# Kernel tuning notes

Hardware: AMD Instinct MI355X
Metric: run time of the kernel (lower is better)

Reference implementation:

```python
import jax, jax.numpy as jnp
import numpy as np

E, HEADS, HD, L, FF = 768, 12, 64, 12, 3072


def layernorm(x, g, b, eps=1e-5):
    m = jnp.mean(x, axis=-1, keepdims=True)
    v = jnp.var(x, axis=-1, keepdims=True)
    return (x - m) / jnp.sqrt(v + eps) * g + b


def setup_inputs() -> dict:
    key = jax.random.key(0)
    ks = jax.random.split(key, 26)
    B, N, PS = 32, 1024, 24
    P2 = PS * PS
    def rn(k, shape, s=0.02):
        return jax.random.normal(k, shape, dtype=jnp.float32) * s
    return {
        "scene_masks": jax.random.normal(ks[0], (B, N, PS, PS), dtype=jnp.float32),
        "target_mask": jax.random.normal(ks[1], (B, PS, PS), dtype=jnp.float32),
        "emb_W": rn(ks[2], (E, P2)),            # torch Linear weight [out,in]
        "emb_b": rn(ks[3], (E,)),
        "class_embed": rn(ks[4], (1, 1, E)),
        "scene_pos": rn(ks[5], (1, N + 1, E)),
        "target_pos": rn(ks[6], (1, 2, E)),
        "ln1_g": jnp.ones((L, E), jnp.float32),
        "ln1_b": jnp.zeros((L, E), jnp.float32),
        "ln2_g": jnp.ones((L, E), jnp.float32),
        "ln2_b": jnp.zeros((L, E), jnp.float32),
        "Wq": rn(ks[7], (L, HD, HD)),
        "Wk": rn(ks[8], (L, HD, HD)),
        "Wv": rn(ks[9], (L, HD, HD)),
        "Wo": rn(ks[10], (L, E, E)),
        "bo": rn(ks[11], (L, E)),
        "W1": rn(ks[12], (L, FF, E)),
        "b1": rn(ks[13], (L, FF)),
        "W2": rn(ks[14], (L, E, FF)),
        "b2": rn(ks[15], (L, E)),
        "mlp_W": rn(ks[16], (N, E)),
        "mlp_b": rn(ks[17], (N,)),
    }


def _forward_logits(scene_masks, target_mask, emb_W, emb_b, class_embed, scene_pos,
                    target_pos, ln1_g, ln1_b, ln2_g, ln2_b, Wq, Wk, Wv, Wo, bo,
                    W1, b1, W2, b2, mlp_W, mlp_b):
    B, N, H, W = scene_masks.shape
    P2 = H * W
    scene = scene_masks.reshape(B, N, P2) @ emb_W.T + emb_b          # [B,N,E]
    tgt = target_mask.reshape(B, 1, P2) @ emb_W.T + emb_b            # [B,1,E]
    cls = jnp.broadcast_to(class_embed, (B, 1, E))
    scene = jnp.concatenate([cls, scene], axis=1) + scene_pos[:, :N + 1]  # [B,N+1,E]
    tgt = jnp.concatenate([cls, tgt], axis=1) + target_pos               # [B,2,E]
    scale = jnp.sqrt(jnp.float32(E))

    def block(tq, p):
        g1, bb1n, g2, bb2n, wq, wk, wv, wo, bo_, w1, b1_, w2, b2_ = p
        kv = layernorm(scene, g1, bb1n)                # norm1(value)=norm1(key)
        q = layernorm(tq, g1, bb1n)                    # norm1(query)
        kvh = kv.reshape(B, N + 1, HEADS, HD)
        qh = q.reshape(B, 2, HEADS, HD)
        # per-head Linear shares one [HD,HD] weight across all heads
        qs = jnp.einsum('nqhd,ed->nqhe', qh, wq)
        ks_ = jnp.einsum('nkhd,ed->nkhe', kvh, wk)
        vs = jnp.einsum('nkhd,ed->nkhe', kvh, wv)
        energy = jnp.einsum('nqhd,nkhd->nhqk', qs, ks_)     # [B,H,2,N+1]
        att = jax.nn.softmax(energy / scale, axis=-1)
        out = jnp.einsum('nhqk,nkhd->nqhd', att, vs).reshape(B, 2, E)
        out = out @ wo.T + bo_
        x = layernorm(out + tq, g1, bb1n)
        ff = jax.nn.relu(x @ w1.T + b1_) @ w2.T + b2_
        return layernorm(ff + x, g2, bb2n), None

    params = (ln1_g, ln1_b, ln2_g, ln2_b, Wq, Wk, Wv, Wo, bo, W1, b1, W2, b2)
    tgt, _ = jax.lax.scan(block, tgt, params)
    x = jnp.mean(tgt, axis=1) @ mlp_W.T + mlp_b       # [B, num_patches]
    return x


def reference(scene_masks, target_mask, emb_W, emb_b, class_embed, scene_pos,
              target_pos, ln1_g, ln1_b, ln2_g, ln2_b, Wq, Wk, Wv, Wo, bo,
              W1, b1, W2, b2, mlp_W, mlp_b):
    x = _forward_logits(scene_masks, target_mask, emb_W, emb_b, class_embed,
                        scene_pos, target_pos, ln1_g, ln1_b, ln2_g, ln2_b,
                        Wq, Wk, Wv, Wo, bo, W1, b1, W2, b2, mlp_W, mlp_b)
    # sorted_nodes = argsort desc + 1; eye(P+1)[nodes-1] == one_hot(argsort desc)
    order = jnp.argsort(-x, axis=1)[:, :5]                # top-5 patch indices
    return jax.nn.one_hot(order, x.shape[1] + 1, dtype=jnp.float32)  # [B,5,P+1]
```

## Files before the change

kernel.cpp:

```cpp
#include <hip/hip_runtime.h>
#include <math.h>

#define E_DIM 768
#define NTOK 1025
#define B_DIM 32
#define NHEADS 12
#define HDIM 64
#define LAYERS 12
#define FF_DIM 3072
#define P2 576

__device__ __forceinline__ float block_reduce_sum(float v, float* red) {
  int tid = threadIdx.x;
  red[tid] = v;
  __syncthreads();
#pragma unroll
  for (int s = 128; s > 0; s >>= 1) {
    if (tid < s) red[tid] += red[tid + s];
    __syncthreads();
  }
  float r = red[0];
  __syncthreads();
  return r;
}

__global__ __launch_bounds__(256) void embed_gemm(
    const float* __restrict__ A, const float* __restrict__ W,
    const float* __restrict__ bias, const float* __restrict__ pos,
    float* __restrict__ scene) {
  __shared__ float Xs[16][132];
  __shared__ float Ws[16][132];
  int tid = threadIdx.x;
  int n0 = blockIdx.x * 128;
  int m0 = blockIdx.y * 128;
  int lr = tid >> 2;
  int lk = (tid & 3) << 2;
  int ty = tid >> 4, tx = tid & 15;
  float acc[8][8] = {};
  for (int k0 = 0; k0 < P2; k0 += 16) {
    float4 x0 = *(const float4*)(A + (size_t)(m0 + lr) * P2 + k0 + lk);
    float4 x1 = *(const float4*)(A + (size_t)(m0 + 64 + lr) * P2 + k0 + lk);
    float4 w0 = *(const float4*)(W + (size_t)(n0 + lr) * P2 + k0 + lk);
    float4 w1 = *(const float4*)(W + (size_t)(n0 + 64 + lr) * P2 + k0 + lk);
    __syncthreads();
    Xs[lk + 0][lr] = x0.x; Xs[lk + 1][lr] = x0.y; Xs[lk + 2][lr] = x0.z; Xs[lk + 3][lr] = x0.w;
    Xs[lk + 0][64 + lr] = x1.x; Xs[lk + 1][64 + lr] = x1.y; Xs[lk + 2][64 + lr] = x1.z; Xs[lk + 3][64 + lr] = x1.w;
    Ws[lk + 0][lr] = w0.x; Ws[lk + 1][lr] = w0.y; Ws[lk + 2][lr] = w0.z; Ws[lk + 3][lr] = w0.w;
    Ws[lk + 0][64 + lr] = w1.x; Ws[lk + 1][64 + lr] = w1.y; Ws[lk + 2][64 + lr] = w1.z; Ws[lk + 3][64 + lr] = w1.w;
    __syncthreads();
#pragma unroll
    for (int kk = 0; kk < 16; ++kk) {
      float4 a0 = *(const float4*)&Xs[kk][ty << 2];
      float4 a1 = *(const float4*)&Xs[kk][64 + (ty << 2)];
      float4 b0 = *(const float4*)&Ws[kk][tx << 2];
      float4 b1 = *(const float4*)&Ws[kk][64 + (tx << 2)];
      float av[8] = {a0.x, a0.y, a0.z, a0.w, a1.x, a1.y, a1.z, a1.w};
      float bv[8] = {b0.x, b0.y, b0.z, b0.w, b1.x, b1.y, b1.z, b1.w};
#pragma unroll
      for (int i = 0; i < 8; ++i)
#pragma unroll
        for (int j = 0; j < 8; ++j) acc[i][j] += av[i] * bv[j];
    }
  }
#pragma unroll
  for (int i = 0; i < 8; ++i) {
    int mloc = (i < 4) ? ((ty << 2) + i) : (64 + (ty << 2) + i - 4);
    int m = m0 + mloc;
    int b = m >> 10, nt = m & 1023;
    size_t row = ((size_t)b * NTOK + 1 + nt) * E_DIM;
    size_t prow = (size_t)(1 + nt) * E_DIM;
#pragma unroll
    for (int half = 0; half < 2; ++half) {
      int n = n0 + half * 64 + (tx << 2);
      float4 o4;
      o4.x = acc[i][half * 4 + 0] + bias[n + 0] + pos[prow + n + 0];
      o4.y = acc[i][half * 4 + 1] + bias[n + 1] + pos[prow + n + 1];
      o4.z = acc[i][half * 4 + 2] + bias[n + 2] + pos[prow + n + 2];
      o4.w = acc[i][half * 4 + 3] + bias[n + 3] + pos[prow + n + 3];
      *(float4*)&scene[row + n] = o4;
    }
  }
}

__global__ void scene_cls(const float* __restrict__ cls, const float* __restrict__ pos,
                          float* __restrict__ scene) {
  int b = blockIdx.x;
  for (int e = threadIdx.x; e < E_DIM; e += 256)
    scene[(size_t)b * NTOK * E_DIM + e] = cls[e] + pos[e];
}

__global__ __launch_bounds__(256) void ln_rows(const float* __restrict__ in, float* __restrict__ out) {
  __shared__ float red[256];
  int r = blockIdx.x, tid = threadIdx.x;
  const float* x = in + (size_t)r * E_DIM;
  float a0 = x[tid], a1 = x[tid + 256], a2 = x[tid + 512];
  float mean = block_reduce_sum(a0 + a1 + a2, red) * (1.f / 768.f);
  float d0 = a0 - mean, d1 = a1 - mean, d2 = a2 - mean;
  float var = block_reduce_sum(d0 * d0 + d1 * d1 + d2 * d2, red) * (1.f / 768.f);
  float rinv = rsqrtf(var + 1e-5f);
  float* o = out + (size_t)r * E_DIM;
  o[tid] = d0 * rinv; o[tid + 256] = d1 * rinv; o[tid + 512] = d2 * rinv;
}

__global__ __launch_bounds__(256) void tgt_init(
    const float* __restrict__ tmask, const float* __restrict__ W,
    const float* __restrict__ bias, const float* __restrict__ cls,
    const float* __restrict__ tpos, float* __restrict__ tq) {
  int b = blockIdx.x, tid = threadIdx.x;
  for (int e = tid; e < E_DIM; e += 256)
    tq[(size_t)(b * 2) * E_DIM + e] = cls[e] + tpos[e];
  const float* tm = tmask + (size_t)b * P2;
  for (int e = tid; e < E_DIM; e += 256) {
    const float* wr = W + (size_t)e * P2;
    float s = 0.f;
    for (int k = 0; k < P2; k += 4) {
      float4 w4 = *(const float4*)&wr[k];
      float4 t4 = *(const float4*)&tm[k];
      s += w4.x * t4.x + w4.y * t4.y + w4.z * t4.z + w4.w * t4.w;
    }
    tq[(size_t)(b * 2 + 1) * E_DIM + e] = s + bias[e] + tpos[E_DIM + e];
  }
}

__global__ void prep_m(const float* __restrict__ Wq, const float* __restrict__ Wk,
                       float* __restrict__ Mb) {
  int l = blockIdx.y;
  int idx = blockIdx.x * 256 + threadIdx.x;
  int d = idx >> 6, dp = idx & 63;
  const float* wq = Wq + l * 4096;
  const float* wk = Wk + l * 4096;
  float s = 0.f;
#pragma unroll 8
  for (int e = 0; e < 64; ++e) s += wq[e * 64 + d] * wk[e * 64 + dp];
  Mb[l * 4096 + idx] = s;
}

__global__ void prep_wvo(const float* __restrict__ Wv, const float* __restrict__ Wo,
                         float* __restrict__ Wvo) {
  int l = blockIdx.y;
  int idx = blockIdx.x * 256 + threadIdx.x;
  int ep = idx / 768, hd = idx % 768;
  int h = hd >> 6, d = hd & 63;
  const float* wv = Wv + (size_t)l * 4096;
  const float* wo = Wo + (size_t)l * 768 * 768 + (size_t)ep * 768 + h * 64;
  float s = 0.f;
#pragma unroll 8
  for (int ev = 0; ev < 64; ++ev) s += wv[ev * 64 + d] * wo[ev];
  Wvo[(size_t)l * 589824 + idx] = s;
}

#define ACH 272
__global__ __launch_bounds__(256) void attn_flash_q(
    const float* __restrict__ tq, const float* __restrict__ Mb,
    const float* __restrict__ g1, const float* __restrict__ b1, int l,
    const float* __restrict__ ns, float* __restrict__ ctx) {
  __shared__ float red[256];
  __shared__ float qs[2][64];
  __shared__ float qg[2][64];
  __shared__ float qmb[2];
  __shared__ float sred[2][16];
  __shared__ float cred[2][16][64];
  int b = blockIdx.x / NHEADS;
  int h = blockIdx.x % NHEADS;
  int tid = threadIdx.x;
  const float* gl = g1 + l * E_DIM;
  const float* bl = b1 + l * E_DIM;
  int seg = h >> 2;
  int base = h * 64 - seg * 256;
  for (int r = 0; r < 2; ++r) {
    const float* x = tq + (size_t)(b * 2 + r) * E_DIM;
    float a0 = x[tid], a1 = x[tid + 256], a2 = x[tid + 512];
    float mean = block_reduce_sum(a0 + a1 + a2, red) * (1.f / 768.f);
    float d0 = a0 - mean, d1 = a1 - mean, d2 = a2 - mean;
    float var = block_reduce_sum(d0 * d0 + d1 * d1 + d2 * d2, red) * (1.f / 768.f);
    float rinv = rsqrtf(var + 1e-5f);
    float dv = (seg == 0) ? d0 : ((seg == 1) ? d1 : d2);
    if (tid >= base && tid < base + 64) {
      int d = tid - base;
      qs[r][d] = dv * rinv * gl[h * 64 + d] + bl[h * 64 + d];
    }
  }
  __syncthreads();
  const float inv_scale = rsqrtf(768.f);
  if (tid < 128) {
    int r = tid >> 6, dp = tid & 63;
    const float* M = Mb + l * 4096;
    float s = 0.f;
#pragma unroll 8
    for (int d = 0; d < 64; ++d) s += qs[r][d] * M[d * 64 + dp];
    qg[r][dp] = s * gl[h * 64 + dp] * inv_scale;
    red[tid] = s * bl[h * 64 + dp];
  }
  __syncthreads();
  if (tid < 2) {
    float a = 0.f;
    for (int dp = 0; dp < 64; ++dp) a += red[tid * 64 + dp];
    qmb[tid] = a * inv_scale;
  }
  __syncthreads();
  int g = tid >> 4;
  int lane = tid & 15;
  int r0 = b * 2, r1 = r0 + 1;
  const float* nsb = ns + (size_t)b * NTOK * E_DIM + h * 64;
  float4 q0v = *(const float4*)&qg[0][lane * 4];
  float4 q1v = *(const float4*)&qg[1][lane * 4];
  float qb0 = qmb[0], qb1 = qmb[1];
  float m = -1e30f, s0 = 0.f, s1 = 0.f;
  float4 c0 = {0, 0, 0, 0}, c1 = {0, 0, 0, 0};
  float4 v[17];
  float e0a[17], e1a[17];
  for (int cb = 0; cb < NTOK; cb += ACH) {
    int ntk = NTOK - cb; if (ntk > ACH) ntk = ACH;
    int cnt = (ntk - g + 15) >> 4;
    float mloc = -1e30f;
#pragma unroll
    for (int i = 0; i < 17; ++i) {
      if (i < cnt) {
        int k = cb + g + (i << 4);
        float4 vv = *(const float4*)(nsb + (size_t)k * E_DIM + lane * 4);
        v[i] = vv;
        float p0 = vv.x * q0v.x + vv.y * q0v.y + vv.z * q0v.z + vv.w * q0v.w;
        float p1 = vv.x * q1v.x + vv.y * q1v.y + vv.z * q1v.z + vv.w * q1v.w;
#pragma unroll
        for (int off = 8; off; off >>= 1) {
          p0 += __shfl_xor(p0, off, 16);
          p1 += __shfl_xor(p1, off, 16);
        }
        float e0 = p0 + qb0, e1 = p1 + qb1;
        e0a[i] = e0; e1a[i] = e1;
        mloc = fmaxf(mloc, fmaxf(e0, e1));
      }
    }
    red[tid] = mloc;
    __syncthreads();
#pragma unroll
    for (int s = 128; s > 0; s >>= 1) {
      if (tid < s) red[tid] = fmaxf(red[tid], red[tid + s]);
      __syncthreads();
    }
    float mnew = fmaxf(m, red[0]);
    __syncthreads();
    if (mnew > m) {
      float f = expf(m - mnew);
      s0 *= f; s1 *= f;
      c0.x *= f; c0.y *= f; c0.z *= f; c0.w *= f;
      c1.x *= f; c1.y *= f; c1.z *= f; c1.w *= f;
      m = mnew;
    }
#pragma unroll
    for (int i = 0; i < 17; ++i) {
      if (i < cnt) {
        float p0 = expf(e0a[i] - m);
        float p1 = expf(e1a[i] - m);
        s0 += p0; s1 += p1;
        c0.x += p0 * v[i].x; c0.y += p0 * v[i].y; c0.z += p0 * v[i].z; c0.w += p0 * v[i].w;
        c1.x += p1 * v[i].x; c1.y += p1 * v[i].y; c1.z += p1 * v[i].z; c1.w += p1 * v[i].w;
      }
    }
  }
  if (lane == 0) { sred[0][g] = s0; sred[1][g] = s1; }
  *(float4*)&cred[0][g][lane * 4] = c0;
  *(float4*)&cred[1][g][lane * 4] = c1;
  __syncthreads();
  if (tid < 128) {
    int t = tid >> 6, dd = tid & 63;
    int o = h * 64 + dd;
    float stot = 0.f, cs = 0.f;
#pragma unroll
    for (int gg = 0; gg < 16; ++gg) { stot += sred[t][gg]; cs += cred[t][gg][dd]; }
    float inv = 1.f / stot;
    ctx[(size_t)(r0 + t) * E_DIM + o] = cs * inv * gl[o] + bl[o];
  }
}

__global__ __launch_bounds__(256) void skinny_part(
    const float* __restrict__ X, int K, const float* __restrict__ W,
    int kchunk, float* __restrict__ part, int N) {
  __shared__ float Xs[16][64];
  __shared__ float Ws[16][64];
  int tid = threadIdx.x;
  int n0 = blockIdx.x * 64;
  int s = blockIdx.y;
  int kbeg = s * kchunk;
  int lr = tid >> 2;
  int lk = (tid & 3) << 2;
  int ty = tid >> 4, tx = tid & 15;
  float acc[4][4] = {};
  for (int k0 = kbeg; k0 < kbeg + kchunk; k0 += 16) {
    float4 xv = *(const float4*)(X + (size_t)lr * K + k0 + lk);
    float4 wv = *(const float4*)(W + (size_t)(n0 + lr) * K + k0 + lk);
    __syncthreads();
    Xs[lk + 0][lr] = xv.x; Xs[lk + 1][lr] = xv.y; Xs[lk + 2][lr] = xv.z; Xs[lk + 3][lr] = xv.w;
    Ws[lk + 0][lr] = wv.x; Ws[lk + 1][lr] = wv.y; Ws[lk + 2][lr] = wv.z; Ws[lk + 3][lr] = wv.w;
    __syncthreads();
#pragma unroll
    for (int kk = 0; kk < 16; ++kk) {
      float4 a4 = *(const float4*)&Xs[kk][ty << 2];
      float4 b4 = *(const float4*)&Ws[kk][tx << 2];
      float av[4] = {a4.x, a4.y, a4.z, a4.w};
      float bv[4] = {b4.x, b4.y, b4.z, b4.w};
#pragma unroll
      for (int i = 0; i < 4; ++i)
#pragma unroll
        for (int j = 0; j < 4; ++j) acc[i][j] += av[i] * bv[j];
    }
  }
#pragma unroll
  for (int i = 0; i < 4; ++i) {
    int mm = (ty << 2) + i;
    float4 o4 = make_float4(acc[i][0], acc[i][1], acc[i][2], acc[i][3]);
    *(float4*)&part[((size_t)s * 64 + mm) * N + n0 + (tx << 2)] = o4;
  }
}

__global__ __launch_bounds__(256) void skinny_h1_part(
    const float* __restrict__ part1, const float* __restrict__ b1,
    const float* __restrict__ W, int kchunk, float* __restrict__ part2) {
  __shared__ float Xs[16][64];
  __shared__ float Ws[16][64];
  const int K = 3072, N = 768;
  int tid = threadIdx.x;
  int n0 = blockIdx.x * 64;
  int s = blockIdx.y;
  int kbeg = s * kchunk;
  int lr = tid >> 2;
  int lk = (tid & 3) << 2;
  int ty = tid >> 4, tx = tid & 15;
  float acc[4][4] = {};
  for (int k0 = kbeg; k0 < kbeg + kchunk; k0 += 16) {
    float4 x0 = *(const float4*)(part1 + (size_t)lr * K + k0 + lk);
    float4 x1 = *(const float4*)(part1 + (size_t)(64 + lr) * K + k0 + lk);
    float4 x2 = *(const float4*)(part1 + (size_t)(128 + lr) * K + k0 + lk);
    float4 x3 = *(const float4*)(part1 + (size_t)(192 + lr) * K + k0 + lk);
    float4 bb = *(const float4*)(b1 + k0 + lk);
    float4 xv;
    xv.x = fmaxf(x0.x + x1.x + x2.x + x3.x + bb.x, 0.f);
    xv.y = fmaxf(x0.y + x1.y + x2.y + x3.y + bb.y, 0.f);
    xv.z = fmaxf(x0.z + x1.z + x2.z + x3.z + bb.z, 0.f);
    xv.w = fmaxf(x0.w + x1.w + x2.w + x3.w + bb.w, 0.f);
    float4 wv = *(const float4*)(W + (size_t)(n0 + lr) * K + k0 + lk);
    __syncthreads();
    Xs[lk + 0][lr] = xv.x; Xs[lk + 1][lr] = xv.y; Xs[lk + 2][lr] = xv.z; Xs[lk + 3][lr] = xv.w;
    Ws[lk + 0][lr] = wv.x; Ws[lk + 1][lr] = wv.y; Ws[lk + 2][lr] = wv.z; Ws[lk + 3][lr] = wv.w;
    __syncthreads();
#pragma unroll
    for (int kk = 0; kk < 16; ++kk) {
      float4 a4 = *(const float4*)&Xs[kk][ty << 2];
      float4 b4 = *(const float4*)&Ws[kk][tx << 2];
      float av[4] = {a4.x, a4.y, a4.z, a4.w};
      float bv[4] = {b4.x, b4.y, b4.z, b4.w};
#pragma unroll
      for (int i = 0; i < 4; ++i)
#pragma unroll
        for (int j = 0; j < 4; ++j) acc[i][j] += av[i] * bv[j];
    }
  }
#pragma unroll
  for (int i = 0; i < 4; ++i) {
    int mm = (ty << 2) + i;
    float4 o4 = make_float4(acc[i][0], acc[i][1], acc[i][2], acc[i][3]);
    *(float4*)&part2[((size_t)s * 64 + mm) * N + n0 + (tx << 2)] = o4;
  }
}

__global__ __launch_bounds__(256) void reduce_ln(
    const float* __restrict__ part, int S, const float* __restrict__ bias,
    const float* __restrict__ res, const float* __restrict__ g,
    const float* __restrict__ bsh, float* __restrict__ out,
    float* __restrict__ xmean) {
  __shared__ float red[256];
  int m = blockIdx.x, tid = threadIdx.x;
  float t[3];
#pragma unroll
  for (int c = 0; c < 3; ++c) {
    int n = tid + c * 256;
    float s = 0.f;
    for (int i = 0; i < S; ++i) s += part[((size_t)i * 64 + m) * 768 + n];
    t[c] = s + bias[n] + res[(size_t)m * 768 + n];
  }
  float mean = block_reduce_sum(t[0] + t[1] + t[2], red) * (1.f / 768.f);
  float d0 = t[0] - mean, d1 = t[1] - mean, d2 = t[2] - mean;
  float var = block_reduce_sum(d0 * d0 + d1 * d1 + d2 * d2, red) * (1.f / 768.f);
  float rinv = rsqrtf(var + 1e-5f);
  float y0 = d0 * rinv * g[tid] + bsh[tid];
  float y1 = d1 * rinv * g[tid + 256] + bsh[tid + 256];
  float y2 = d2 * rinv * g[tid + 512] + bsh[tid + 512];
  out[(size_t)m * 768 + tid] = y0;
  out[(size_t)m * 768 + tid + 256] = y1;
  out[(size_t)m * 768 + tid + 512] = y2;
  if (xmean) {
    float* xr = xmean + (size_t)(m >> 1) * 768;
    atomicAdd(&xr[tid], 0.5f * y0);
    atomicAdd(&xr[tid + 256], 0.5f * y1);
    atomicAdd(&xr[tid + 512], 0.5f * y2);
  }
}

__global__ __launch_bounds__(256) void top5_from_parts(
    const float* __restrict__ part, const float* __restrict__ bias,
    float* __restrict__ out) {
  __shared__ float v[1024];
  __shared__ float bv[256];
  __shared__ int bi[256];
  int b = blockIdx.x, tid = threadIdx.x;
  for (int i = tid; i < 1024; i += 256) {
    float s = part[(size_t)(0 * 64 + b) * 1024 + i] + part[(size_t)(1 * 64 + b) * 1024 + i] +
              part[(size_t)(2 * 64 + b) * 1024 + i] + part[(size_t)(3 * 64 + b) * 1024 + i];
    v[i] = s + bias[i];
  }
  float* ob = out + (size_t)b * 5 * NTOK;
  for (int i = tid; i < 5 * NTOK; i += 256) ob[i] = 0.f;
  __syncthreads();
  for (int it = 0; it < 5; ++it) {
    float best = -1e38f;
    int bidx = 0x7fffffff;
    for (int i = tid; i < 1024; i += 256) {
      float x = v[i];
      if (x > best || (x == best && i < bidx)) { best = x; bidx = i; }
    }
    bv[tid] = best; bi[tid] = bidx;
    __syncthreads();
    for (int s = 128; s > 0; s >>= 1) {
      if (tid < s) {
        if (bv[tid + s] > bv[tid] || (bv[tid + s] == bv[tid] && bi[tid + s] < bi[tid])) {
          bv[tid] = bv[tid + s]; bi[tid] = bi[tid + s];
        }
      }
      __syncthreads();
    }
    if (tid == 0) {
      ob[it * NTOK + bi[0]] = 1.0f;
      v[bi[0]] = -1e38f;
    }
    __syncthreads();
  }
}

extern "C" void kernel_launch(void* const* d_in, const int* in_sizes, int n_in,
                              void* d_out, int out_size, void* d_ws, size_t ws_size,
                              hipStream_t stream) {
  const float* scene_masks = (const float*)d_in[0];
  const float* target_mask = (const float*)d_in[1];
  const float* emb_W = (const float*)d_in[2];
  const float* emb_b = (const float*)d_in[3];
  const float* class_embed = (const float*)d_in[4];
  const float* scene_pos = (const float*)d_in[5];
  const float* target_pos = (const float*)d_in[6];
  const float* ln1_g = (const float*)d_in[7];
  const float* ln1_b = (const float*)d_in[8];
  const float* ln2_g = (const float*)d_in[9];
  const float* ln2_b = (const float*)d_in[10];
  const float* Wq = (const float*)d_in[11];
  const float* Wk = (const float*)d_in[12];
  const float* Wv = (const float*)d_in[13];
  const float* Wo = (const float*)d_in[14];
  const float* bo = (const float*)d_in[15];
  const float* W1 = (const float*)d_in[16];
  const float* fb1 = (const float*)d_in[17];
  const float* W2 = (const float*)d_in[18];
  const float* fb2 = (const float*)d_in[19];
  const float* mlp_W = (const float*)d_in[20];
  const float* mlp_b = (const float*)d_in[21];
  float* out = (float*)d_out;

  float* ws = (float*)d_ws;
  float* scene = ws;
  float* Mbuf = scene + 25190400;
  float* Wvo = Mbuf + 49152;
  float* tq = Wvo + 7077888;
  float* ctxf = tq + 49152;
  float* xbuf = ctxf + 49152;
  float* xm = xbuf + 49152;
  float* partA = xm + 49152;
  float* partB = partA + 786432;

  embed_gemm<<<dim3(6, 256), 256, 0, stream>>>(scene_masks, emb_W, emb_b, scene_pos, scene);
  scene_cls<<<32, 256, 0, stream>>>(class_embed, scene_pos, scene);
  ln_rows<<<32 * NTOK, 256, 0, stream>>>(scene, scene);
  tgt_init<<<32, 256, 0, stream>>>(target_mask, emb_W, emb_b, class_embed, target_pos, tq);
  prep_m<<<dim3(16, 12), 256, 0, stream>>>(Wq, Wk, Mbuf);
  prep_wvo<<<dim3(2304, 12), 256, 0, stream>>>(Wv, Wo, Wvo);
  hipMemsetAsync(xm, 0, 49152 * sizeof(float), stream);

  for (int l = 0; l < LAYERS; ++l) {
    attn_flash_q<<<32 * NHEADS, 256, 0, stream>>>(tq, Mbuf, ln1_g, ln1_b, l, scene, ctxf);
    skinny_part<<<dim3(12, 8), 256, 0, stream>>>(ctxf, 768, Wvo + (size_t)l * 589824, 96, partA, 768);
    reduce_ln<<<64, 256, 0, stream>>>(partA, 8, bo + l * 768, tq,
                                      ln1_g + l * 768, ln1_b + l * 768, xbuf, nullptr);
    skinny_part<<<dim3(48, 4), 256, 0, stream>>>(xbuf, 768, W1 + (size_t)l * FF_DIM * 768, 192, partB, FF_DIM);
    skinny_h1_part<<<dim3(12, 16), 256, 0, stream>>>(partB, fb1 + l * FF_DIM,
                                                     W2 + (size_t)l * 768 * FF_DIM, 192, partA);
    reduce_ln<<<64, 256, 0, stream>>>(partA, 16, fb2 + l * 768, xbuf,
                                      ln2_g + l * 768, ln2_b + l * 768, tq,
                                      (l == LAYERS - 1) ? xm : nullptr);
  }

  skinny_part<<<dim3(16, 4), 256, 0, stream>>>(xm, 768, mlp_W, 192, partA, 1024);
  top5_from_parts<<<32, 256, 0, stream>>>(partA, mlp_b, out);
}
```

Baseline: 1.931 ms.

## Fuse Wvo projection into attention and replace split-K partials with atomic accumulators

The attention kernel now projects its per-head context through the combined Wvo matrix itself and atomically adds the result into an accumulator. That accumulator is pre-seeded with the residual plus output bias. The second FFN GEMM also accumulates with atomics into a buffer pre-seeded with the residual plus bias. This removes one skinny GEMM launch per layer and the partial-sum reduction passes. In exchange it adds atomic contention, makes float summation order nondeterministic, and has each attention block re-read a slice of Wvo.

```diff
diff --git a/kernel.cpp b/kernel.cpp
--- a/kernel.cpp
+++ b/kernel.cpp
@@ -105,10 +105,14 @@
 __global__ __launch_bounds__(256) void tgt_init(
     const float* __restrict__ tmask, const float* __restrict__ W,
     const float* __restrict__ bias, const float* __restrict__ cls,
-    const float* __restrict__ tpos, float* __restrict__ tq) {
+    const float* __restrict__ tpos, const float* __restrict__ bo0,
+    float* __restrict__ tq, float* __restrict__ acc1) {
   int b = blockIdx.x, tid = threadIdx.x;
-  for (int e = tid; e < E_DIM; e += 256)
-    tq[(size_t)(b * 2) * E_DIM + e] = cls[e] + tpos[e];
+  for (int e = tid; e < E_DIM; e += 256) {
+    float v = cls[e] + tpos[e];
+    tq[(size_t)(b * 2) * E_DIM + e] = v;
+    acc1[(size_t)(b * 2) * E_DIM + e] = v + bo0[e];
+  }
   const float* tm = tmask + (size_t)b * P2;
   for (int e = tid; e < E_DIM; e += 256) {
     const float* wr = W + (size_t)e * P2;
@@ -118,7 +122,9 @@
       float4 t4 = *(const float4*)&tm[k];
       s += w4.x * t4.x + w4.y * t4.y + w4.z * t4.z + w4.w * t4.w;
     }
-    tq[(size_t)(b * 2 + 1) * E_DIM + e] = s + bias[e] + tpos[E_DIM + e];
+    float v = s + bias[e] + tpos[E_DIM + e];
+    tq[(size_t)(b * 2 + 1) * E_DIM + e] = v;
+    acc1[(size_t)(b * 2 + 1) * E_DIM + e] = v + bo0[e];
   }
 }
 
@@ -153,13 +159,15 @@
 __global__ __launch_bounds__(256) void attn_flash_q(
     const float* __restrict__ tq, const float* __restrict__ Mb,
     const float* __restrict__ g1, const float* __restrict__ b1, int l,
-    const float* __restrict__ ns, float* __restrict__ ctx) {
+    const float* __restrict__ ns, const float* __restrict__ Wvo_l,
+    float* __restrict__ acc1) {
   __shared__ float red[256];
   __shared__ float qs[2][64];
   __shared__ float qg[2][64];
   __shared__ float qmb[2];
   __shared__ float sred[2][16];
   __shared__ float cred[2][16][64];
+  __shared__ float ctxs[2][64];
   int b = blockIdx.x / NHEADS;
   int h = blockIdx.x % NHEADS;
   int tid = threadIdx.x;
@@ -269,8 +277,49 @@
 #pragma unroll
     for (int gg = 0; gg < 16; ++gg) { stot += sred[t][gg]; cs += cred[t][gg][dd]; }
     float inv = 1.f / stot;
-    ctx[(size_t)(r0 + t) * E_DIM + o] = cs * inv * gl[o] + bl[o];
-  }
+    ctxs[t][dd] = cs * inv * gl[o] + bl[o];
+  }
+  __syncthreads();
+  const float* wbase = Wvo_l + (size_t)h * 64 + lane * 4;
+  float4 x0 = *(const float4*)&ctxs[0][lane * 4];
+  float4 x1 = *(const float4*)&ctxs[1][lane * 4];
+  for (int n = g; n < 768; n += 16) {
+    float4 wv = *(const float4*)(wbase + (size_t)n * 768);
+    float a0 = wv.x * x0.x + wv.y * x0.y + wv.z * x0.z + wv.w * x0.w;
+    float a1 = wv.x * x1.x + wv.y * x1.y + wv.z * x1.z + wv.w * x1.w;
+#pragma unroll
+    for (int off = 8; off; off >>= 1) {
+      a0 += __shfl_xor(a0, off, 16);
+      a1 += __shfl_xor(a1, off, 16);
+    }
+    if (lane == 0) {
+      atomicAdd(&acc1[(size_t)r0 * E_DIM + n], a0);
+      atomicAdd(&acc1[(size_t)r1 * E_DIM + n], a1);
+    }
+  }
+}
+
+__global__ __launch_bounds__(256) void ln1_ff2init(
+    const float* __restrict__ acc1, const float* __restrict__ g,
+    const float* __restrict__ bsh, const float* __restrict__ fb2l,
+    float* __restrict__ x, float* __restrict__ acc2) {
+  __shared__ float red[256];
+  int m = blockIdx.x, tid = threadIdx.x;
+  const float* a = acc1 + (size_t)m * E_DIM;
+  float t0 = a[tid], t1 = a[tid + 256], t2 = a[tid + 512];
+  float mean = block_reduce_sum(t0 + t1 + t2, red) * (1.f / 768.f);
+  float d0 = t0 - mean, d1 = t1 - mean, d2 = t2 - mean;
+  float var = block_reduce_sum(d0 * d0 + d1 * d1 + d2 * d2, red) * (1.f / 768.f);
+  float rinv = rsqrtf(var + 1e-5f);
+  float y0 = d0 * rinv * g[tid] + bsh[tid];
+  float y1 = d1 * rinv * g[tid + 256] + bsh[tid + 256];
+  float y2 = d2 * rinv * g[tid + 512] + bsh[tid + 512];
+  x[(size_t)m * E_DIM + tid] = y0;
+  x[(size_t)m * E_DIM + tid + 256] = y1;
+  x[(size_t)m * E_DIM + tid + 512] = y2;
+  acc2[(size_t)m * E_DIM + tid] = y0 + fb2l[tid];
+  acc2[(size_t)m * E_DIM + tid + 256] = y1 + fb2l[tid + 256];
+  acc2[(size_t)m * E_DIM + tid + 512] = y2 + fb2l[tid + 512];
 }
 
 __global__ __launch_bounds__(256) void skinny_part(
@@ -313,9 +362,9 @@
   }
 }
 
-__global__ __launch_bounds__(256) void skinny_h1_part(
+__global__ __launch_bounds__(256) void skinny_h1_atomic(
     const float* __restrict__ part1, const float* __restrict__ b1,
-    const float* __restrict__ W, int kchunk, float* __restrict__ part2) {
+    const float* __restrict__ W, int kchunk, float* __restrict__ acc2) {
   __shared__ float Xs[16][64];
   __shared__ float Ws[16][64];
   const int K = 3072, N = 768;
@@ -358,38 +407,40 @@
 #pragma unroll
   for (int i = 0; i < 4; ++i) {
     int mm = (ty << 2) + i;
-    float4 o4 = make_float4(acc[i][0], acc[i][1], acc[i][2], acc[i][3]);
-    *(float4*)&part2[((size_t)s * 64 + mm) * N + n0 + (tx << 2)] = o4;
-  }
-}
-
-__global__ __launch_bounds__(256) void reduce_ln(
-    const float* __restrict__ part, int S, const float* __restrict__ bias,
-    const float* __restrict__ res, const float* __restrict__ g,
-    const float* __restrict__ bsh, float* __restrict__ out,
+    float* dst = acc2 + (size_t)mm * N + n0 + (tx << 2);
+    atomicAdd(dst + 0, acc[i][0]);
+    atomicAdd(dst + 1, acc[i][1]);
+    atomicAdd(dst + 2, acc[i][2]);
+    atomicAdd(dst + 3, acc[i][3]);
+  }
+}
+
+__global__ __launch_bounds__(256) void ln2_next(
+    const float* __restrict__ acc2, const float* __restrict__ g,
+    const float* __restrict__ bsh, const float* __restrict__ bo_next,
+    float* __restrict__ tq, float* __restrict__ acc1,
     float* __restrict__ xmean) {
   __shared__ float red[256];
   int m = blockIdx.x, tid = threadIdx.x;
-  float t[3];
-#pragma unroll
-  for (int c = 0; c < 3; ++c) {
-    int n = tid + c * 256;
-    float s = 0.f;
-    for (int i = 0; i < S; ++i) s += part[((size_t)i * 64 + m) * 768 + n];
-    t[c] = s + bias[n] + res[(size_t)m * 768 + n];
-  }
-  float mean = block_reduce_sum(t[0] + t[1] + t[2], red) * (1.f / 768.f);
-  float d0 = t[0] - mean, d1 = t[1] - mean, d2 = t[2] - mean;
+  const float* a = acc2 + (size_t)m * E_DIM;
+  float t0 = a[tid], t1 = a[tid + 256], t2 = a[tid + 512];
+  float mean = block_reduce_sum(t0 + t1 + t2, red) * (1.f / 768.f);
+  float d0 = t0 - mean, d1 = t1 - mean, d2 = t2 - mean;
   float var = block_reduce_sum(d0 * d0 + d1 * d1 + d2 * d2, red) * (1.f / 768.f);
   float rinv = rsqrtf(var + 1e-5f);
   float y0 = d0 * rinv * g[tid] + bsh[tid];
   float y1 = d1 * rinv * g[tid + 256] + bsh[tid + 256];
   float y2 = d2 * rinv * g[tid + 512] + bsh[tid + 512];
-  out[(size_t)m * 768 + tid] = y0;
-  out[(size_t)m * 768 + tid + 256] = y1;
-  out[(size_t)m * 768 + tid + 512] = y2;
+  tq[(size_t)m * E_DIM + tid] = y0;
+  tq[(size_t)m * E_DIM + tid + 256] = y1;
+  tq[(size_t)m * E_DIM + tid + 512] = y2;
+  if (bo_next) {
+    acc1[(size_t)m * E_DIM + tid] = y0 + bo_next[tid];
+    acc1[(size_t)m * E_DIM + tid + 256] = y1 + bo_next[tid + 256];
+    acc1[(size_t)m * E_DIM + tid + 512] = y2 + bo_next[tid + 512];
+  }
   if (xmean) {
-    float* xr = xmean + (size_t)(m >> 1) * 768;
+    float* xr = xmean + (size_t)(m >> 1) * E_DIM;
     atomicAdd(&xr[tid], 0.5f * y0);
     atomicAdd(&xr[tid + 256], 0.5f * y1);
     atomicAdd(&xr[tid + 512], 0.5f * y2);
@@ -468,31 +519,34 @@
   float* Mbuf = scene + 25190400;
   float* Wvo = Mbuf + 49152;
   float* tq = Wvo + 7077888;
-  float* ctxf = tq + 49152;
-  float* xbuf = ctxf + 49152;
-  float* xm = xbuf + 49152;
+  float* xbuf = tq + 49152;
+  float* acc1 = xbuf + 49152;
+  float* acc2 = acc1 + 49152;
+  float* xm = acc2 + 49152;
   float* partA = xm + 49152;
   float* partB = partA + 786432;
 
   embed_gemm<<<dim3(6, 256), 256, 0, stream>>>(scene_masks, emb_W, emb_b, scene_pos, scene);
   scene_cls<<<32, 256, 0, stream>>>(class_embed, scene_pos, scene);
   ln_rows<<<32 * NTOK, 256, 0, stream>>>(scene, scene);
-  tgt_init<<<32, 256, 0, stream>>>(target_mask, emb_W, emb_b, class_embed, target_pos, tq);
+  tgt_init<<<32, 256, 0, stream>>>(target_mask, emb_W, emb_b, class_embed, target_pos,
+                                   bo, tq, acc1);
   prep_m<<<dim3(16, 12), 256, 0, stream>>>(Wq, Wk, Mbuf);
   prep_wvo<<<dim3(2304, 12), 256, 0, stream>>>(Wv, Wo, Wvo);
   hipMemsetAsync(xm, 0, 49152 * sizeof(float), stream);
 
   for (int l = 0; l < LAYERS; ++l) {
-    attn_flash_q<<<32 * NHEADS, 256, 0, stream>>>(tq, Mbuf, ln1_g, ln1_b, l, scene, ctxf);
-    skinny_part<<<dim3(12, 8), 256, 0, stream>>>(ctxf, 768, Wvo + (size_t)l * 589824, 96, partA, 768);
-    reduce_ln<<<64, 256, 0, stream>>>(partA, 8, bo + l * 768, tq,
-                                      ln1_g + l * 768, ln1_b + l * 768, xbuf, nullptr);
+    attn_flash_q<<<32 * NHEADS, 256, 0, stream>>>(tq, Mbuf, ln1_g, ln1_b, l, scene,
+                                                  Wvo + (size_t)l * 589824, acc1);
+    ln1_ff2init<<<64, 256, 0, stream>>>(acc1, ln1_g + l * 768, ln1_b + l * 768,
+                                        fb2 + l * 768, xbuf, acc2);
     skinny_part<<<dim3(48, 4), 256, 0, stream>>>(xbuf, 768, W1 + (size_t)l * FF_DIM * 768, 192, partB, FF_DIM);
-    skinny_h1_part<<<dim3(12, 16), 256, 0, stream>>>(partB, fb1 + l * FF_DIM,
-                                                     W2 + (size_t)l * 768 * FF_DIM, 192, partA);
-    reduce_ln<<<64, 256, 0, stream>>>(partA, 16, fb2 + l * 768, xbuf,
-                                      ln2_g + l * 768, ln2_b + l * 768, tq,
-                                      (l == LAYERS - 1) ? xm : nullptr);
+    skinny_h1_atomic<<<dim3(12, 16), 256, 0, stream>>>(partB, fb1 + l * FF_DIM,
+                                                       W2 + (size_t)l * 768 * FF_DIM, 192, acc2);
+    ln2_next<<<64, 256, 0, stream>>>(acc2, ln2_g + l * 768, ln2_b + l * 768,
+                                     (l < LAYERS - 1) ? (bo + (l + 1) * 768) : nullptr,
+                                     tq, acc1,
+                                     (l == LAYERS - 1) ? xm : nullptr);
   }
 
   skinny_part<<<dim3(16, 4), 256, 0, stream>>>(xm, 768, mlp_W, 192, partA, 1024);
```

Measured after the change: 2.070 ms. 7.2% more time.
